# Optimization experiments

Hardware: AMD Instinct MI355X
Metric: run time of the kernel (lower is better)

## Reference

```python
import jax, jax.numpy as jnp
import numpy as np

EPS = 1e-6

def setup_inputs() -> dict:
    key = jax.random.key(0)
    ks = jax.random.split(key, 4)
    T, B, D, N = 512, 16, 1024, 512
    # xavier-uniform-ish scale for projections
    lim = float(np.sqrt(6.0 / (N + D)))
    x = jax.random.normal(ks[0], (T, B, D), dtype=jnp.float32)
    W_k = jax.random.uniform(ks[1], (N, D), minval=-lim, maxval=lim, dtype=jnp.float32)
    W_v = jax.random.uniform(ks[2], (N, D), minval=-lim, maxval=lim, dtype=jnp.float32)
    W_q = jax.random.uniform(ks[3], (N, D), minval=-lim, maxval=lim, dtype=jnp.float32)
    return {"x": x, "W_k": W_k, "W_v": W_v, "W_q": W_q}

def reference(x, W_k, W_v, W_q):
    # x: (T, B, D); delta-rule fast-weight cell, proj=no_z, nonlin=tanh,
    # gate=output, update=delta.
    T, B, D = x.shape
    n = W_k.shape[0]
    k = jnp.einsum('tbd,nd->tbn', x, W_k)
    v = jnp.einsum('tbd,nd->tbn', x, W_v)
    q = jnp.einsum('tbd,nd->tbn', x, W_q)
    k_norm = k / (jnp.linalg.norm(k, axis=-1, keepdims=True) + EPS)

    def step(S, kvq):
        k_t, v_t, q_t = kvq  # each (B, n)
        retrieved = jnp.einsum('bij,bj->bi', S, k_t)
        delta = v_t - retrieved
        S_new = jnp.tanh(S + delta[:, :, None] * k_t[:, None, :])
        Sq = jnp.einsum('bij,bj->bi', S_new, q_t)
        out = Sq * jax.nn.silu(Sq)
        return S_new, out

    S0 = jnp.zeros((B, n, n), dtype=x.dtype)
    S_final, outputs = jax.lax.scan(step, S0, (k_norm, v, q))
    return outputs, S_final
```

## Files before the change

kernel.cpp:

```cpp
#include <hip/hip_runtime.h>
#include <hip/hip_bf16.h>

#define T_DIM 512
#define B_DIM 16
#define D_DIM 1024
#define N_DIM 512

#define C_FOLD  2.885390082f
#define INV_C   0.3465735903f

typedef short s16x8 __attribute__((ext_vector_type(8)));
typedef float f32x4 __attribute__((ext_vector_type(4)));
typedef float f32x2 __attribute__((ext_vector_type(2)));

__device__ __forceinline__ unsigned cvt2bf(float lo, float hi) {
    unsigned r;
    asm("v_cvt_pk_bf16_f32 %0, %1, %2" : "=v"(r) : "v"(lo), "v"(hi));
    return r;
}

__device__ __forceinline__ float reduce16(float x) {
    x += __int_as_float(__builtin_amdgcn_update_dpp(0, __float_as_int(x), 0xB1,  0xf, 0xf, true));
    x += __int_as_float(__builtin_amdgcn_update_dpp(0, __float_as_int(x), 0x4E,  0xf, 0xf, true));
    x += __int_as_float(__builtin_amdgcn_update_dpp(0, __float_as_int(x), 0x124, 0xf, 0xf, true));
    x += __int_as_float(__builtin_amdgcn_update_dpp(0, __float_as_int(x), 0x128, 0xf, 0xf, true));
    return x;
}

__global__ __launch_bounds__(256) void proj_gemm(
    const float* __restrict__ x,
    const float* __restrict__ Wk,
    const float* __restrict__ Wv,
    const float* __restrict__ Wq,
    float* __restrict__ kbuf, float* __restrict__ vbuf, float* __restrict__ qbuf)
{
    __shared__ __align__(16) unsigned short As[64 * 40];
    __shared__ __align__(16) unsigned short Bk[64 * 40];
    __shared__ __align__(16) unsigned short Bv[64 * 40];
    __shared__ __align__(16) unsigned short Bq[64 * 40];

    const int tid  = threadIdx.x;
    const int m0   = blockIdx.x * 64;
    const int n0   = blockIdx.y * 64;
    const int wave = tid >> 6;
    const int lane = tid & 63;
    const int l15  = lane & 15;
    const int quad = lane >> 4;

    const int srow = tid >> 2;
    const int scol = (tid & 3) * 8;

    f32x4 ak[4], av[4], aq[4];
#pragma unroll
    for (int i = 0; i < 4; ++i) { ak[i] = (f32x4)0.0f; av[i] = (f32x4)0.0f; aq[i] = (f32x4)0.0f; }

    const size_t aoff = (size_t)(m0 + srow) * D_DIM + scol;
    const size_t boff = (size_t)(n0 + srow) * D_DIM + scol;

    for (int k0 = 0; k0 < D_DIM; k0 += 32) {
        __syncthreads();
        {
            const float* srcA = &x[aoff + k0];
            float4 a0 = *(const float4*)srcA;
            float4 a1 = *(const float4*)(srcA + 4);
            uint4 pa;
            pa.x = cvt2bf(a0.x, a0.y);
            pa.y = cvt2bf(a0.z, a0.w);
            pa.z = cvt2bf(a1.x, a1.y);
            pa.w = cvt2bf(a1.z, a1.w);
            *(uint4*)&As[srow * 40 + scol] = pa;

            const float* sk = &Wk[boff + k0];
            float4 b0 = *(const float4*)sk;
            float4 b1 = *(const float4*)(sk + 4);
            uint4 pb;
            pb.x = cvt2bf(b0.x, b0.y);
            pb.y = cvt2bf(b0.z, b0.w);
            pb.z = cvt2bf(b1.x, b1.y);
            pb.w = cvt2bf(b1.z, b1.w);
            *(uint4*)&Bk[srow * 40 + scol] = pb;

            const float* sv = &Wv[boff + k0];
            b0 = *(const float4*)sv;
            b1 = *(const float4*)(sv + 4);
            pb.x = cvt2bf(b0.x, b0.y);
            pb.y = cvt2bf(b0.z, b0.w);
            pb.z = cvt2bf(b1.x, b1.y);
            pb.w = cvt2bf(b1.z, b1.w);
            *(uint4*)&Bv[srow * 40 + scol] = pb;

            const float* sq = &Wq[boff + k0];
            b0 = *(const float4*)sq;
            b1 = *(const float4*)(sq + 4);
            pb.x = cvt2bf(b0.x, b0.y);
            pb.y = cvt2bf(b0.z, b0.w);
            pb.z = cvt2bf(b1.x, b1.y);
            pb.w = cvt2bf(b1.z, b1.w);
            *(uint4*)&Bq[srow * 40 + scol] = pb;
        }
        __syncthreads();
        s16x8 af = *(const s16x8*)&As[(wave * 16 + l15) * 40 + quad * 8];
#pragma unroll
        for (int nt = 0; nt < 4; ++nt) {
            s16x8 bk = *(const s16x8*)&Bk[(nt * 16 + l15) * 40 + quad * 8];
            ak[nt] = __builtin_amdgcn_mfma_f32_16x16x32_bf16(af, bk, ak[nt], 0, 0, 0);
            s16x8 bv = *(const s16x8*)&Bv[(nt * 16 + l15) * 40 + quad * 8];
            av[nt] = __builtin_amdgcn_mfma_f32_16x16x32_bf16(af, bv, av[nt], 0, 0, 0);
            s16x8 bq = *(const s16x8*)&Bq[(nt * 16 + l15) * 40 + quad * 8];
            aq[nt] = __builtin_amdgcn_mfma_f32_16x16x32_bf16(af, bq, aq[nt], 0, 0, 0);
        }
    }
#pragma unroll
    for (int nt = 0; nt < 4; ++nt) {
#pragma unroll
        for (int rg = 0; rg < 4; ++rg) {
            int row = m0 + wave * 16 + quad * 4 + rg;
            int col = n0 + nt * 16 + l15;
            kbuf[(size_t)row * N_DIM + col] = ak[nt][rg];
            vbuf[(size_t)row * N_DIM + col] = av[nt][rg];
            qbuf[(size_t)row * N_DIM + col] = aq[nt][rg];
        }
    }
}

__global__ __launch_bounds__(256) void knorm(float* __restrict__ kbuf)
{
    const int wave = threadIdx.x >> 6;
    const int lane = threadIdx.x & 63;
    const int row  = blockIdx.x * 4 + wave;
    float* p = &kbuf[(size_t)row * N_DIM + lane * 8];
    float4 a = *(const float4*)p;
    float4 b = *(const float4*)(p + 4);
    float s = a.x*a.x + a.y*a.y + a.z*a.z + a.w*a.w
            + b.x*b.x + b.y*b.y + b.z*b.z + b.w*b.w;
#pragma unroll
    for (int m = 1; m < 64; m <<= 1) s += __shfl_xor(s, m, 64);
    float inv = 1.0f / (sqrtf(s) + 1e-6f);
    a.x *= inv; a.y *= inv; a.z *= inv; a.w *= inv;
    b.x *= inv; b.y *= inv; b.z *= inv; b.w *= inv;
    *(float4*)p = a;
    *(float4*)(p + 4) = b;
}

__global__ __launch_bounds__(256, 2) void scan_kernel(
    const float* __restrict__ kbuf, const float* __restrict__ vbuf,
    const float* __restrict__ qbuf, float* __restrict__ out)
{
    __shared__ __align__(16) float ks[2][576];
    __shared__ __align__(16) float qs[2][576];
    __shared__ float vs[2][16];

    const int tid = threadIdx.x;
    const int l4  = tid & 15;
    const int g   = tid >> 4;
    const int b   = blockIdx.y;
    const int i0  = blockIdx.x * 16;

    const int wA  = 36 * (tid >> 4) + ((2 * tid) & 31);
    const int rA2 = 36 * l4;

    f32x2 S2[16];
#pragma unroll
    for (int u = 0; u < 16; ++u) S2[u] = (f32x2)0.0f;

    const int DT = B_DIM * N_DIM;
    const float* kp = kbuf + (size_t)b * N_DIM + 2 * tid;
    const float* qp = qbuf + (size_t)b * N_DIM + 2 * tid;
    const float* vp = vbuf + (size_t)b * N_DIM + i0 + tid;

    float2 pk, pq; float pv = 0.0f;
    {
        pk = *(const float2*)kp; kp += DT;
        pq = *(const float2*)qp; qp += DT;
        if (tid < 16) pv = *vp;
        vp += DT;
        *(float2*)&ks[0][wA] = pk;
        *(float2*)&qs[0][wA] = pq;
        if (tid < 16) vs[0][tid] = pv;
        pk = *(const float2*)kp; kp += DT;
        pq = *(const float2*)qp; qp += DT;
        if (tid < 16) pv = *vp;
        vp += DT;
    }
    __syncthreads();

    float* op = out + (size_t)b * N_DIM + i0 + g;

    const f32x2 Cv   = {C_FOLD, C_FOLD};
    const f32x2 M2Cv = {-2.0f * C_FOLD, -2.0f * C_FOLD};

    for (int t = 0; t < T_DIM; ++t) {
        const int cb = t & 1, nb = cb ^ 1;

        if (t + 1 < T_DIM) {
            *(float2*)&ks[nb][wA] = pk;
            *(float2*)&qs[nb][wA] = pq;
            if (tid < 16) vs[nb][tid] = pv;
        }
        if (t + 2 < T_DIM) {
            pk = *(const float2*)kp;
            pq = *(const float2*)qp;
            if (tid < 16) pv = *vp;
        }
        kp += DT; qp += DT; vp += DT;

        f32x4 kk[8];
#pragma unroll
        for (int u = 0; u < 8; ++u)
            kk[u] = *(const f32x4*)&ks[cb][rA2 + 4 * u];
        const float v0 = vs[cb][g];

        f32x2 p0 = (f32x2)0.0f, p1 = (f32x2)0.0f;
        f32x2 p2 = (f32x2)0.0f, p3 = (f32x2)0.0f;
#pragma unroll
        for (int u = 0; u < 8; u += 2) {
            p0 += S2[2*u]     * kk[u].xy;
            p1 += S2[2*u + 1] * kk[u].zw;
            p2 += S2[2*u + 2] * kk[u + 1].xy;
            p3 += S2[2*u + 3] * kk[u + 1].zw;
        }
        p0 += p1; p2 += p3; p0 += p2;
        const float racc = reduce16(p0.x + p0.y);

        const float dp = __builtin_fmaf(C_FOLD, v0, -racc);
        const f32x2 d0 = {dp, dp};

        f32x2 sacc0 = (f32x2)0.0f, sacc1 = (f32x2)0.0f;
#pragma unroll
        for (int w = 0; w < 4; ++w) {
            f32x4 qq0 = *(const f32x4*)&qs[cb][rA2 + 8 * w];
            f32x4 qq1 = *(const f32x4*)&qs[cb][rA2 + 8 * w + 4];
            f32x2 a0 = S2[4*w]     + d0 * kk[2*w].xy;
            f32x2 a1 = S2[4*w + 1] + d0 * kk[2*w].zw;
            f32x2 a2 = S2[4*w + 2] + d0 * kk[2*w + 1].xy;
            f32x2 a3 = S2[4*w + 3] + d0 * kk[2*w + 1].zw;
            f32x2 f0 = { __builtin_amdgcn_exp2f(a0.x), __builtin_amdgcn_exp2f(a0.y) };
            f32x2 f1 = { __builtin_amdgcn_exp2f(a1.x), __builtin_amdgcn_exp2f(a1.y) };
            f32x2 f2 = { __builtin_amdgcn_exp2f(a2.x), __builtin_amdgcn_exp2f(a2.y) };
            f32x2 f3 = { __builtin_amdgcn_exp2f(a3.x), __builtin_amdgcn_exp2f(a3.y) };
            f0 = f0 + 1.0f; f1 = f1 + 1.0f; f2 = f2 + 1.0f; f3 = f3 + 1.0f;
            f32x2 m0 = f0 * f1;
            f32x2 m1 = f2 * f3;
            f32x2 qqp = m0 * m1;
            float rP = __builtin_amdgcn_rcpf(qqp.x * qqp.y);
            f32x2 rq  = { qqp.y * rP, qqp.x * rP };
            f32x2 rm0 = rq * m1;
            f32x2 rm1 = rq * m0;
            f32x2 r0 = rm0 * f1;
            f32x2 r1 = rm0 * f0;
            f32x2 r2 = rm1 * f3;
            f32x2 r3 = rm1 * f2;
            f32x2 n0 = Cv + r0 * M2Cv;
            f32x2 n1 = Cv + r1 * M2Cv;
            f32x2 n2 = Cv + r2 * M2Cv;
            f32x2 n3 = Cv + r3 * M2Cv;
            S2[4*w] = n0; S2[4*w + 1] = n1; S2[4*w + 2] = n2; S2[4*w + 3] = n3;
            sacc0 += n0 * qq0.xy + n2 * qq1.xy;
            sacc1 += n1 * qq0.zw + n3 * qq1.zw;
        }
        sacc0 += sacc1;
        const float sq = reduce16(sacc0.x + sacc0.y);

        if (l4 == 0) {
            float s0 = sq * INV_C;
            float g0 = __builtin_amdgcn_rcpf(1.0f + __builtin_amdgcn_exp2f(-s0 * 1.44269504f));
            op[0] = s0 * s0 * g0;
        }
        op += DT;
        __syncthreads();
    }

    const size_t base = (size_t)T_DIM * B_DIM * N_DIM;
    const size_t so = base + ((size_t)b * N_DIM + i0 + g) * N_DIM + 32 * l4;
#pragma unroll
    for (int u = 0; u < 8; ++u) {
        float4 w0;
        w0.x = S2[2*u].x   * INV_C; w0.y = S2[2*u].y   * INV_C;
        w0.z = S2[2*u+1].x * INV_C; w0.w = S2[2*u+1].y * INV_C;
        *(float4*)&out[so + 4 * u] = w0;
    }
}

extern "C" void kernel_launch(void* const* d_in, const int* in_sizes, int n_in,
                              void* d_out, int out_size, void* d_ws, size_t ws_size,
                              hipStream_t stream) {
    const float* x  = (const float*)d_in[0];
    const float* Wk = (const float*)d_in[1];
    const float* Wv = (const float*)d_in[2];
    const float* Wq = (const float*)d_in[3];
    float* outp = (float*)d_out;

    const size_t MN = (size_t)T_DIM * B_DIM * N_DIM;
    float* kbuf = (float*)d_ws;
    float* vbuf = kbuf + MN;
    float* qbuf = vbuf + MN;

    proj_gemm<<<dim3(128, 8), 256, 0, stream>>>(x, Wk, Wv, Wq, kbuf, vbuf, qbuf);
    knorm<<<2048, 256, 0, stream>>>(kbuf);
    scan_kernel<<<dim3(32, 16), 256, 0, stream>>>(kbuf, vbuf, qbuf, outp);
}
```

Before: 708.1 us.

## Load k/q directly from global into registers, drop LDS staging and barriers

Each thread now reads its k and q slices straight from global memory into registers, using a strided column mapping (4*l4 + 64*u), and no longer stages them through double-buffered shared memory. This removes the per-step __syncthreads and the LDS writes and reads. Loads for the next step are double-buffered in registers by unrolling the time loop by two. The trade-off is redundant global/L2 traffic, since all 16 row-groups load the same k/q, and higher register pressure from holding two sets of k/q vectors.

```diff
diff --git a/kernel.cpp b/kernel.cpp
--- a/kernel.cpp
+++ b/kernel.cpp
@@ -146,138 +146,125 @@
     const float* __restrict__ kbuf, const float* __restrict__ vbuf,
     const float* __restrict__ qbuf, float* __restrict__ out)
 {
-    __shared__ __align__(16) float ks[2][576];
-    __shared__ __align__(16) float qs[2][576];
-    __shared__ float vs[2][16];
-
     const int tid = threadIdx.x;
     const int l4  = tid & 15;
     const int g   = tid >> 4;
     const int b   = blockIdx.y;
     const int i0  = blockIdx.x * 16;
 
-    const int wA  = 36 * (tid >> 4) + ((2 * tid) & 31);
-    const int rA2 = 36 * l4;
-
     f32x2 S2[16];
 #pragma unroll
     for (int u = 0; u < 16; ++u) S2[u] = (f32x2)0.0f;
 
     const int DT = B_DIM * N_DIM;
-    const float* kp = kbuf + (size_t)b * N_DIM + 2 * tid;
-    const float* qp = qbuf + (size_t)b * N_DIM + 2 * tid;
-    const float* vp = vbuf + (size_t)b * N_DIM + i0 + tid;
-
-    float2 pk, pq; float pv = 0.0f;
-    {
-        pk = *(const float2*)kp; kp += DT;
-        pq = *(const float2*)qp; qp += DT;
-        if (tid < 16) pv = *vp;
-        vp += DT;
-        *(float2*)&ks[0][wA] = pk;
-        *(float2*)&qs[0][wA] = pq;
-        if (tid < 16) vs[0][tid] = pv;
-        pk = *(const float2*)kp; kp += DT;
-        pq = *(const float2*)qp; qp += DT;
-        if (tid < 16) pv = *vp;
-        vp += DT;
-    }
-    __syncthreads();
-
+    const float* kp = kbuf + (size_t)b * N_DIM + 4 * l4;
+    const float* qp = qbuf + (size_t)b * N_DIM + 4 * l4;
+    const float* vp = vbuf + (size_t)b * N_DIM + i0 + g;
     float* op = out + (size_t)b * N_DIM + i0 + g;
 
     const f32x2 Cv   = {C_FOLD, C_FOLD};
     const f32x2 M2Cv = {-2.0f * C_FOLD, -2.0f * C_FOLD};
 
-    for (int t = 0; t < T_DIM; ++t) {
-        const int cb = t & 1, nb = cb ^ 1;
-
-        if (t + 1 < T_DIM) {
-            *(float2*)&ks[nb][wA] = pk;
-            *(float2*)&qs[nb][wA] = pq;
-            if (tid < 16) vs[nb][tid] = pv;
-        }
+    f32x4 kA[8], qA[8]; float vA;
+    f32x4 kB[8], qB[8]; float vB;
+
+#pragma unroll
+    for (int u = 0; u < 8; ++u) {
+        kA[u] = *(const f32x4*)(kp + 64 * u);
+        qA[u] = *(const f32x4*)(qp + 64 * u);
+    }
+    vA = *vp;
+    kp += DT; qp += DT; vp += DT;
+
+#define SCAN_STEP(KK, QQ, VV)                                                 \
+    {                                                                         \
+        f32x2 p0 = (f32x2)0.0f, p1 = (f32x2)0.0f;                             \
+        f32x2 p2 = (f32x2)0.0f, p3 = (f32x2)0.0f;                             \
+        _Pragma("unroll")                                                     \
+        for (int u = 0; u < 8; u += 2) {                                      \
+            p0 += S2[2*u]     * KK[u].xy;                                     \
+            p1 += S2[2*u + 1] * KK[u].zw;                                     \
+            p2 += S2[2*u + 2] * KK[u + 1].xy;                                 \
+            p3 += S2[2*u + 3] * KK[u + 1].zw;                                 \
+        }                                                                     \
+        p0 += p1; p2 += p3; p0 += p2;                                         \
+        const float racc = reduce16(p0.x + p0.y);                             \
+        const float dp = __builtin_fmaf(C_FOLD, VV, -racc);                   \
+        const f32x2 d0 = {dp, dp};                                            \
+        f32x2 sacc0 = (f32x2)0.0f, sacc1 = (f32x2)0.0f;                       \
+        _Pragma("unroll")                                                     \
+        for (int w = 0; w < 4; ++w) {                                         \
+            f32x2 a0 = S2[4*w]     + d0 * KK[2*w].xy;                         \
+            f32x2 a1 = S2[4*w + 1] + d0 * KK[2*w].zw;                         \
+            f32x2 a2 = S2[4*w + 2] + d0 * KK[2*w + 1].xy;                     \
+            f32x2 a3 = S2[4*w + 3] + d0 * KK[2*w + 1].zw;                     \
+            f32x2 f0 = { __builtin_amdgcn_exp2f(a0.x), __builtin_amdgcn_exp2f(a0.y) }; \
+            f32x2 f1 = { __builtin_amdgcn_exp2f(a1.x), __builtin_amdgcn_exp2f(a1.y) }; \
+            f32x2 f2 = { __builtin_amdgcn_exp2f(a2.x), __builtin_amdgcn_exp2f(a2.y) }; \
+            f32x2 f3 = { __builtin_amdgcn_exp2f(a3.x), __builtin_amdgcn_exp2f(a3.y) }; \
+            f0 = f0 + 1.0f; f1 = f1 + 1.0f; f2 = f2 + 1.0f; f3 = f3 + 1.0f;   \
+            f32x2 m0 = f0 * f1;                                               \
+            f32x2 m1 = f2 * f3;                                               \
+            f32x2 qq = m0 * m1;                                               \
+            float rP = __builtin_amdgcn_rcpf(qq.x * qq.y);                    \
+            f32x2 rq  = { qq.y * rP, qq.x * rP };                             \
+            f32x2 rm0 = rq * m1;                                              \
+            f32x2 rm1 = rq * m0;                                              \
+            f32x2 r0 = rm0 * f1;                                              \
+            f32x2 r1 = rm0 * f0;                                              \
+            f32x2 r2 = rm1 * f3;                                              \
+            f32x2 r3 = rm1 * f2;                                              \
+            f32x2 n0 = Cv + r0 * M2Cv;                                        \
+            f32x2 n1 = Cv + r1 * M2Cv;                                        \
+            f32x2 n2 = Cv + r2 * M2Cv;                                        \
+            f32x2 n3 = Cv + r3 * M2Cv;                                        \
+            S2[4*w] = n0; S2[4*w + 1] = n1; S2[4*w + 2] = n2; S2[4*w + 3] = n3; \
+            sacc0 += n0 * QQ[2*w].xy + n2 * QQ[2*w + 1].xy;                   \
+            sacc1 += n1 * QQ[2*w].zw + n3 * QQ[2*w + 1].zw;                   \
+        }                                                                     \
+        sacc0 += sacc1;                                                       \
+        const float sq = reduce16(sacc0.x + sacc0.y);                         \
+        if (l4 == 0) {                                                        \
+            float s0 = sq * INV_C;                                            \
+            float g0 = __builtin_amdgcn_rcpf(1.0f + __builtin_amdgcn_exp2f(-s0 * 1.44269504f)); \
+            op[0] = s0 * s0 * g0;                                             \
+        }                                                                     \
+        op += DT;                                                             \
+    }
+
+    for (int t = 0; t < T_DIM; t += 2) {
+#pragma unroll
+        for (int u = 0; u < 8; ++u) {
+            kB[u] = *(const f32x4*)(kp + 64 * u);
+            qB[u] = *(const f32x4*)(qp + 64 * u);
+        }
+        vB = *vp;
+        kp += DT; qp += DT; vp += DT;
+
+        SCAN_STEP(kA, qA, vA);
+
         if (t + 2 < T_DIM) {
-            pk = *(const float2*)kp;
-            pq = *(const float2*)qp;
-            if (tid < 16) pv = *vp;
+#pragma unroll
+            for (int u = 0; u < 8; ++u) {
+                kA[u] = *(const f32x4*)(kp + 64 * u);
+                qA[u] = *(const f32x4*)(qp + 64 * u);
+            }
+            vA = *vp;
         }
         kp += DT; qp += DT; vp += DT;
 
-        f32x4 kk[8];
-#pragma unroll
-        for (int u = 0; u < 8; ++u)
-            kk[u] = *(const f32x4*)&ks[cb][rA2 + 4 * u];
-        const float v0 = vs[cb][g];
-
-        f32x2 p0 = (f32x2)0.0f, p1 = (f32x2)0.0f;
-        f32x2 p2 = (f32x2)0.0f, p3 = (f32x2)0.0f;
-#pragma unroll
-        for (int u = 0; u < 8; u += 2) {
-            p0 += S2[2*u]     * kk[u].xy;
-            p1 += S2[2*u + 1] * kk[u].zw;
-            p2 += S2[2*u + 2] * kk[u + 1].xy;
-            p3 += S2[2*u + 3] * kk[u + 1].zw;
-        }
-        p0 += p1; p2 += p3; p0 += p2;
-        const float racc = reduce16(p0.x + p0.y);
-
-        const float dp = __builtin_fmaf(C_FOLD, v0, -racc);
-        const f32x2 d0 = {dp, dp};
-
-        f32x2 sacc0 = (f32x2)0.0f, sacc1 = (f32x2)0.0f;
-#pragma unroll
-        for (int w = 0; w < 4; ++w) {
-            f32x4 qq0 = *(const f32x4*)&qs[cb][rA2 + 8 * w];
-            f32x4 qq1 = *(const f32x4*)&qs[cb][rA2 + 8 * w + 4];
-            f32x2 a0 = S2[4*w]     + d0 * kk[2*w].xy;
-            f32x2 a1 = S2[4*w + 1] + d0 * kk[2*w].zw;
-            f32x2 a2 = S2[4*w + 2] + d0 * kk[2*w + 1].xy;
-            f32x2 a3 = S2[4*w + 3] + d0 * kk[2*w + 1].zw;
-            f32x2 f0 = { __builtin_amdgcn_exp2f(a0.x), __builtin_amdgcn_exp2f(a0.y) };
-            f32x2 f1 = { __builtin_amdgcn_exp2f(a1.x), __builtin_amdgcn_exp2f(a1.y) };
-            f32x2 f2 = { __builtin_amdgcn_exp2f(a2.x), __builtin_amdgcn_exp2f(a2.y) };
-            f32x2 f3 = { __builtin_amdgcn_exp2f(a3.x), __builtin_amdgcn_exp2f(a3.y) };
-            f0 = f0 + 1.0f; f1 = f1 + 1.0f; f2 = f2 + 1.0f; f3 = f3 + 1.0f;
-            f32x2 m0 = f0 * f1;
-            f32x2 m1 = f2 * f3;
-            f32x2 qqp = m0 * m1;
-            float rP = __builtin_amdgcn_rcpf(qqp.x * qqp.y);
-            f32x2 rq  = { qqp.y * rP, qqp.x * rP };
-            f32x2 rm0 = rq * m1;
-            f32x2 rm1 = rq * m0;
-            f32x2 r0 = rm0 * f1;
-            f32x2 r1 = rm0 * f0;
-            f32x2 r2 = rm1 * f3;
-            f32x2 r3 = rm1 * f2;
-            f32x2 n0 = Cv + r0 * M2Cv;
-            f32x2 n1 = Cv + r1 * M2Cv;
-            f32x2 n2 = Cv + r2 * M2Cv;
-            f32x2 n3 = Cv + r3 * M2Cv;
-            S2[4*w] = n0; S2[4*w + 1] = n1; S2[4*w + 2] = n2; S2[4*w + 3] = n3;
-            sacc0 += n0 * qq0.xy + n2 * qq1.xy;
-            sacc1 += n1 * qq0.zw + n3 * qq1.zw;
-        }
-        sacc0 += sacc1;
-        const float sq = reduce16(sacc0.x + sacc0.y);
-
-        if (l4 == 0) {
-            float s0 = sq * INV_C;
-            float g0 = __builtin_amdgcn_rcpf(1.0f + __builtin_amdgcn_exp2f(-s0 * 1.44269504f));
-            op[0] = s0 * s0 * g0;
-        }
-        op += DT;
-        __syncthreads();
-    }
+        SCAN_STEP(kB, qB, vB);
+    }
+#undef SCAN_STEP
 
     const size_t base = (size_t)T_DIM * B_DIM * N_DIM;
-    const size_t so = base + ((size_t)b * N_DIM + i0 + g) * N_DIM + 32 * l4;
+    const size_t so = base + ((size_t)b * N_DIM + i0 + g) * N_DIM + 4 * l4;
 #pragma unroll
     for (int u = 0; u < 8; ++u) {
         float4 w0;
         w0.x = S2[2*u].x   * INV_C; w0.y = S2[2*u].y   * INV_C;
         w0.z = S2[2*u+1].x * INV_C; w0.w = S2[2*u+1].y * INV_C;
-        *(float4*)&out[so + 4 * u] = w0;
+        *(float4*)&out[so + 64 * u] = w0;
     }
 }
 
```

New measurement: 732.9 us. 3.5% more time.
